# Kernel optimization log

Hardware: AMD Instinct MI355X
Metric: run time of the kernel (lower is better)

Reference implementation:

```python
import jax, jax.numpy as jnp
import numpy as np

N = 50000      # nodes
E = 800000     # edges
H = 64         # num_hidden
NUM_LAYERS = 4 # -> NUM_LAYERS-1 shared-weight processor steps
EPS = 1e-12


def _mlp3(x, w1, b1, w2, b2, w3, b3):
    h = jax.nn.relu(x @ w1 + b1)
    h = jax.nn.relu(h @ w2 + b2)
    return h @ w3 + b3


def setup_inputs() -> dict:
    key = jax.random.key(0)
    ks = jax.random.split(key, 32)

    def gl(k, shape):
        fan_in = shape[0]
        return (jax.random.normal(k, shape, jnp.float32) / np.sqrt(fan_in)).astype(jnp.float32)

    inp = {
        "X_curr": jax.random.normal(ks[0], (N, 6), jnp.float32),
        "y_prev": jax.random.normal(ks[1], (N,), jnp.float32),
        "edge": jax.random.randint(ks[2], (2, E), 0, N, dtype=jnp.int64),
        # edge net: Linear(9,H) ReLU Linear(H,H) ReLU Linear(H,3)
        "ew1": gl(ks[3], (9, H)), "eb1": jnp.zeros((H,), jnp.float32),
        "ew2": gl(ks[4], (H, H)), "eb2": jnp.zeros((H,), jnp.float32),
        "ew3": gl(ks[5], (H, 3)), "eb3": jnp.zeros((3,), jnp.float32),
        # node net: Linear(5,H) ReLU Linear(H,H) ReLU Linear(H,1)
        "nw1": gl(ks[6], (5, H)), "nb1": jnp.zeros((H,), jnp.float32),
        "nw2": gl(ks[7], (H, H)), "nb2": jnp.zeros((H,), jnp.float32),
        "nw3": gl(ks[8], (H, 1)), "nb3": jnp.zeros((1,), jnp.float32),
        # decoder: Linear(5,H) ReLU Linear(H,H) ReLU Linear(H,H) ReLU Linear(H,1)
        "dw1": gl(ks[9], (5, H)),  "db1": jnp.zeros((H,), jnp.float32),
        "dw2": gl(ks[10], (H, H)), "db2": jnp.zeros((H,), jnp.float32),
        "dw3": gl(ks[11], (H, H)), "db3": jnp.zeros((H,), jnp.float32),
        "dw4": gl(ks[12], (H, 1)), "db4": jnp.zeros((1,), jnp.float32),
        "mode": 0,
    }
    return inp


def reference(X_curr, y_prev, edge,
              ew1, eb1, ew2, eb2, ew3, eb3,
              nw1, nb1, nw2, nb2, nw3, nb3,
              dw1, db1, dw2, db2, dw3, db3, dw4, db4,
              mode):
    src, dst = edge[0], edge[1]
    n = X_curr.shape[0]

    # x_in: [N,5] = (pos x,y,z, feature col 4, y_prev)
    x_in = jnp.concatenate([X_curr[:, jnp.array([0, 1, 2, 4])], y_prev[:, None]], axis=-1)

    # initial edge_attr = (f_dest - f_src) * disp  -> [E,3]
    disp0 = x_in[dst, :3] - x_in[src, :3]
    f_r = x_in[dst, 4] - x_in[src, 4]
    edge_attr = f_r[:, None] * disp0

    cnt = jax.ops.segment_sum(jnp.ones((edge.shape[1], 1), x_in.dtype), dst, num_segments=n)
    denom = jnp.maximum(cnt, 1.0)

    for _ in range(NUM_LAYERS - 1):  # shared weights across processors
        xs = x_in[src]
        xd = x_in[dst]
        disp = xd[:, :3] - xs[:, :3]
        norm = jnp.sqrt(jnp.sum(disp * disp, axis=-1, keepdims=True) + EPS)
        net_in = jnp.concatenate([disp, norm, edge_attr, xs[:, 4:5], xd[:, 4:5]], axis=-1)  # [E,9]
        edge_attr = edge_attr + _mlp3(net_in, ew1, eb1, ew2, eb2, ew3, eb3)

        # scatter-mean of edge_attr at destination nodes
        aggr = jax.ops.segment_sum(edge_attr, dst, num_segments=n) / denom  # [N,3]
        node_in = jnp.concatenate([x_in[:, 3:5], aggr], axis=-1)            # [N,5]
        delta = _mlp3(node_in, nw1, nb1, nw2, nb2, nw3, nb3)[:, 0]
        x_in = jnp.concatenate([x_in[:, :4], (x_in[:, 4] + delta)[:, None]], axis=-1)

    # decoder
    h = jax.nn.relu(x_in @ dw1 + db1)
    h = jax.nn.relu(h @ dw2 + db2)
    h = jax.nn.relu(h @ dw3 + db3)
    x_out = h @ dw4 + db4  # [N,1]
    return y_prev + x_out[:, 0]
```

## Files before the change

kernel.cpp:

```cpp
#include <hip/hip_runtime.h>
#include <math.h>

#define N_NODES 50000
#define N_EDGES 800000
#define EPS 1e-12f
#define SCAN_NB 196
#define MAXB 6144

typedef __attribute__((ext_vector_type(8))) short bf16x8;
typedef __attribute__((ext_vector_type(4))) float f32x4;

__device__ inline unsigned pk_bf16(float a, float b) {
    unsigned ua = __float_as_uint(a), ub = __float_as_uint(b);
    ua = (ua + 0x7FFFu + ((ua >> 16) & 1u)) >> 16;
    ub = (ub + 0x7FFFu + ((ub >> 16) & 1u)) >> 16;
    return ua | (ub << 16);
}
__device__ inline unsigned short bf16_1(float a) {
    unsigned ua = __float_as_uint(a);
    return (unsigned short)((ua + 0x7FFFu + ((ua >> 16) & 1u)) >> 16);
}

__global__ void k_node_init(const float* __restrict__ X, const float* __restrict__ yp,
                            float4* __restrict__ px4, float* __restrict__ f) {
    int n = blockIdx.x * blockDim.x + threadIdx.x;
    if (n < N_NODES) {
        px4[n] = make_float4(X[n * 6 + 0], X[n * 6 + 1], X[n * 6 + 2], X[n * 6 + 4]);
        f[n] = yp[n];
    }
}

__global__ __launch_bounds__(256) void k_bucket(const int* __restrict__ edge,
                                                int* __restrict__ btail,
                                                int2* __restrict__ staging) {
    __shared__ int hist[256], loff[256], gbase[256], fill[256];
    __shared__ int2 ebL[2048];
    __shared__ unsigned short bktL[2048];
    const int t = threadIdx.x;
    const int base = blockIdx.x * 2048;
    const int cnt = min(2048, N_EDGES - base);
    hist[t] = 0; fill[t] = 0;
    __syncthreads();

    int2 my[8]; int mb[8];
#pragma unroll
    for (int j = 0; j < 8; j++) {
        int i = base + t + j * 256;
        if (i < N_EDGES) {
            int s = edge[i], d = edge[N_EDGES + i];
            my[j] = make_int2(s, d);
            mb[j] = d >> 8;
            atomicAdd(&hist[mb[j]], 1);
        } else mb[j] = -1;
    }
    __syncthreads();
    int v = hist[t];
    loff[t] = v;
    __syncthreads();
    for (int off = 1; off < 256; off <<= 1) {
        int x = (t >= off) ? loff[t - off] : 0;
        __syncthreads();
        loff[t] += x;
        __syncthreads();
    }
    int ex = loff[t] - v;
    __syncthreads();
    loff[t] = ex;
    if (v > 0) gbase[t] = atomicAdd(&btail[t], v);
    __syncthreads();
#pragma unroll
    for (int j = 0; j < 8; j++) {
        if (mb[j] >= 0) {
            int lp = loff[mb[j]] + atomicAdd(&fill[mb[j]], 1);
            ebL[lp] = my[j];
            bktL[lp] = (unsigned short)mb[j];
        }
    }
    __syncthreads();
    for (int i = t; i < cnt; i += 256) {
        int b = bktL[i];
        int gp = gbase[b] + (i - loff[b]);
        if (gp < MAXB) staging[b * MAXB + gp] = ebL[i];
    }
}

__global__ void k_bscan(const int* __restrict__ btail, int* __restrict__ bbase) {
    __shared__ int s[256];
    int t = threadIdx.x;
    int v = (t < SCAN_NB) ? btail[t] : 0;
    s[t] = v;
    __syncthreads();
    for (int off = 1; off < 256; off <<= 1) {
        int x = (t >= off) ? s[t - off] : 0;
        __syncthreads();
        s[t] += x;
        __syncthreads();
    }
    if (t < SCAN_NB) bbase[t] = s[t] - v;
}

__global__ __launch_bounds__(256) void k_bsort(const int2* __restrict__ staging,
                                               const int* __restrict__ btail,
                                               const int* __restrict__ bbase,
                                               int2* __restrict__ sd,
                                               int* __restrict__ rowptr) {
    __shared__ int hist[256], excl[256], fill[256], sbuf[256];
    __shared__ int2 ebL[MAXB];
    const int b = blockIdx.x, t = threadIdx.x;
    const int size = min(btail[b], MAXB);
    const int gb = bbase[b];
    for (int i = t; i < size; i += 256) ebL[i] = staging[b * MAXB + i];
    hist[t] = 0; fill[t] = 0;
    __syncthreads();
    for (int i = t; i < size; i += 256) atomicAdd(&hist[ebL[i].y & 255], 1);
    __syncthreads();
    int v = hist[t];
    sbuf[t] = v;
    __syncthreads();
    for (int off = 1; off < 256; off <<= 1) {
        int x = (t >= off) ? sbuf[t - off] : 0;
        __syncthreads();
        sbuf[t] += x;
        __syncthreads();
    }
    int ex = sbuf[t] - v;
    excl[t] = ex;
    int n = (b << 8) + t;
    if (n < N_NODES) rowptr[n] = gb + ex;
    if (b == SCAN_NB - 1 && t == 0) rowptr[N_NODES] = N_EDGES;
    __syncthreads();
    for (int i = t; i < size; i += 256) {
        int2 v2 = ebL[i];
        int ld = v2.y & 255;
        int pos = excl[ld] + atomicAdd(&fill[ld], 1);
        sd[gb + pos] = v2;
    }
}

__global__ void k_edge_init(const int2* __restrict__ sd,
                            const float4* __restrict__ px4,
                            const float* __restrict__ yp,
                            float4* __restrict__ dnrm, float4* __restrict__ ea) {
    int e = blockIdx.x * blockDim.x + threadIdx.x;
    if (e < N_EDGES) {
        int2 SD = sd[e];
        float4 ps = px4[SD.x], pd = px4[SD.y];
        float dx = pd.x - ps.x, dy = pd.y - ps.y, dz = pd.z - ps.z;
        float nrm = sqrtf(dx * dx + dy * dy + dz * dz + EPS);
        dnrm[e] = make_float4(dx, dy, dz, nrm);
        float fr = yp[SD.y] - yp[SD.x];
        ea[e] = make_float4(fr * dx, fr * dy, fr * dz, 0.f);
    }
}

#define W1OFF 0
#define W2OFF 4096
#define W3OFF 13312
#define BUFOFF 15616
#define RS 144

__global__ __launch_bounds__(256, 2) void k_edge_mlp(
    const int2* __restrict__ sd, const float4* __restrict__ dnrm,
    float4* __restrict__ ea, const float* __restrict__ f,
    const float* __restrict__ ew1, const float* __restrict__ eb1,
    const float* __restrict__ ew2, const float* __restrict__ eb2,
    const float* __restrict__ ew3, const float* __restrict__ eb3) {
    __shared__ __align__(16) char smem[15616 + 4 * 64 * RS];
    const int t = threadIdx.x;
    const int lane = t & 63, wave = t >> 6;
    const int c = lane & 15, q = lane >> 4;

    {
        int n = t & 63, kg = t >> 6;
        unsigned pk[4];
#pragma unroll
        for (int i = 0; i < 4; i++) {
            int k0 = kg * 8 + i * 2;
            float v0 = (k0 < 9) ? ew1[k0 * 64 + n] : 0.f;
            float v1 = (k0 + 1 < 9) ? ew1[(k0 + 1) * 64 + n] : 0.f;
            pk[i] = pk_bf16(v0, v1);
        }
        *(uint4*)(smem + W1OFF + n * 64 + kg * 16) =
            make_uint4(pk[0], pk[1], pk[2], pk[3]);

        unsigned pk2[8];
#pragma unroll
        for (int i = 0; i < 8; i++) {
            int k0 = kg * 16 + i * 2;
            pk2[i] = pk_bf16(ew2[k0 * 64 + n], ew2[(k0 + 1) * 64 + n]);
        }
        *(uint4*)(smem + W2OFF + n * RS + kg * 32) =
            make_uint4(pk2[0], pk2[1], pk2[2], pk2[3]);
        *(uint4*)(smem + W2OFF + n * RS + kg * 32 + 16) =
            make_uint4(pk2[4], pk2[5], pk2[6], pk2[7]);

        int n3 = t & 15, kg3 = t >> 4;
        unsigned pk3[2];
#pragma unroll
        for (int i = 0; i < 2; i++) {
            int k0 = kg3 * 4 + i * 2;
            float v0 = (n3 < 3) ? ew3[k0 * 3 + n3] : 0.f;
            float v1 = (n3 < 3) ? ew3[(k0 + 1) * 3 + n3] : 0.f;
            pk3[i] = pk_bf16(v0, v1);
        }
        *(uint2*)(smem + W3OFF + n3 * RS + kg3 * 8) = make_uint2(pk3[0], pk3[1]);
    }

    char* mybuf = smem + BUFOFF + wave * (64 * RS);
    const int e = blockIdx.x * 256 + t;
    int2 SD = sd[e];
    float4 DN = dnrm[e];
    float4 EA = ea[e];
    float fs = f[SD.x], fd = f[SD.y];
    {
        char* row = mybuf + lane * RS;
        *(uint4*)(row) = make_uint4(pk_bf16(DN.x, DN.y), pk_bf16(DN.z, DN.w),
                                    pk_bf16(EA.x, EA.y), pk_bf16(EA.z, fs));
        *(uint4*)(row + 16) = make_uint4(pk_bf16(fd, 0.f), 0u, 0u, 0u);
        *(uint4*)(row + 32) = make_uint4(0u, 0u, 0u, 0u);
        *(uint4*)(row + 48) = make_uint4(0u, 0u, 0u, 0u);
    }
    __syncthreads();

    {
        bf16x8 A1[4], B1[4];
#pragma unroll
        for (int mt = 0; mt < 4; mt++)
            A1[mt] = *(bf16x8*)(mybuf + (mt * 16 + c) * RS + q * 16);
#pragma unroll
        for (int nt = 0; nt < 4; nt++)
            B1[nt] = *(bf16x8*)(smem + W1OFF + (nt * 16 + c) * 64 + q * 16);
        f32x4 acc[16];
#pragma unroll
        for (int nt = 0; nt < 4; nt++) {
            float b = eb1[nt * 16 + c];
#pragma unroll
            for (int mt = 0; mt < 4; mt++) acc[mt * 4 + nt] = (f32x4){b, b, b, b};
        }
#pragma unroll
        for (int mt = 0; mt < 4; mt++)
#pragma unroll
            for (int nt = 0; nt < 4; nt++)
                acc[mt * 4 + nt] = __builtin_amdgcn_mfma_f32_16x16x32_bf16(
                    A1[mt], B1[nt], acc[mt * 4 + nt], 0, 0, 0);
#pragma unroll
        for (int mt = 0; mt < 4; mt++)
#pragma unroll
            for (int nt = 0; nt < 4; nt++)
#pragma unroll
                for (int r = 0; r < 4; r++)
                    *(unsigned short*)(mybuf + (mt * 16 + q * 4 + r) * RS +
                                       (nt * 16 + c) * 2) =
                        bf16_1(fmaxf(acc[mt * 4 + nt][r], 0.f));
    }

    bf16x8 B2[8], B3[2];
#pragma unroll
    for (int nt = 0; nt < 4; nt++)
#pragma unroll
        for (int ks = 0; ks < 2; ks++)
            B2[nt * 2 + ks] =
                *(bf16x8*)(smem + W2OFF + (nt * 16 + c) * RS + ks * 64 + q * 16);
#pragma unroll
    for (int ks = 0; ks < 2; ks++)
        B3[ks] = *(bf16x8*)(smem + W3OFF + c * RS + ks * 64 + q * 16);
    float b3i = (c < 3) ? eb3[c] : 0.f;

#pragma unroll
    for (int mt = 0; mt < 4; mt++) {
        bf16x8 A2[2];
#pragma unroll
        for (int ks = 0; ks < 2; ks++)
            A2[ks] = *(bf16x8*)(mybuf + (mt * 16 + c) * RS + ks * 64 + q * 16);
        f32x4 a2[4];
#pragma unroll
        for (int nt = 0; nt < 4; nt++) {
            float b = eb2[nt * 16 + c];
            a2[nt] = (f32x4){b, b, b, b};
            a2[nt] = __builtin_amdgcn_mfma_f32_16x16x32_bf16(A2[0], B2[nt * 2 + 0],
                                                             a2[nt], 0, 0, 0);
            a2[nt] = __builtin_amdgcn_mfma_f32_16x16x32_bf16(A2[1], B2[nt * 2 + 1],
                                                             a2[nt], 0, 0, 0);
        }
#pragma unroll
        for (int nt = 0; nt < 4; nt++)
#pragma unroll
            for (int r = 0; r < 4; r++)
                *(unsigned short*)(mybuf + (mt * 16 + q * 4 + r) * RS +
                                   (nt * 16 + c) * 2) =
                    bf16_1(fmaxf(a2[nt][r], 0.f));
        bf16x8 A3[2];
#pragma unroll
        for (int ks = 0; ks < 2; ks++)
            A3[ks] = *(bf16x8*)(mybuf + (mt * 16 + c) * RS + ks * 64 + q * 16);
        f32x4 a3 = (f32x4){b3i, b3i, b3i, b3i};
        a3 = __builtin_amdgcn_mfma_f32_16x16x32_bf16(A3[0], B3[0], a3, 0, 0, 0);
        a3 = __builtin_amdgcn_mfma_f32_16x16x32_bf16(A3[1], B3[1], a3, 0, 0, 0);
        if (c < 3) {
#pragma unroll
            for (int r = 0; r < 4; r++)
                *(float*)(mybuf + (mt * 16 + q * 4 + r) * RS + 128 + c * 4) = a3[r];
        }
    }

    float4 o = *(float4*)(mybuf + lane * RS + 128);
    ea[e] = make_float4(EA.x + o.x, EA.y + o.y, EA.z + o.z, 0.f);
}

__global__ __launch_bounds__(256, 2) void k_node_mlp(
    const float4* __restrict__ px4, float* __restrict__ f,
    const float4* __restrict__ ea, const int* __restrict__ rowptr,
    const float* __restrict__ nw1, const float* __restrict__ nb1,
    const float* __restrict__ nw2, const float* __restrict__ nb2,
    const float* __restrict__ nw3, const float* __restrict__ nb3) {
    __shared__ __align__(16) char smem[15616 + 4 * 64 * RS];
    const int t = threadIdx.x;
    const int lane = t & 63, wave = t >> 6;
    const int c = lane & 15, q = lane >> 4;

    {
        int n = t & 63, kg = t >> 6;
        unsigned pk[4];
#pragma unroll
        for (int i = 0; i < 4; i++) {
            int k0 = kg * 8 + i * 2;
            float v0 = (k0 < 5) ? nw1[k0 * 64 + n] : 0.f;
            float v1 = (k0 + 1 < 5) ? nw1[(k0 + 1) * 64 + n] : 0.f;
            pk[i] = pk_bf16(v0, v1);
        }
        *(uint4*)(smem + W1OFF + n * 64 + kg * 16) =
            make_uint4(pk[0], pk[1], pk[2], pk[3]);

        unsigned pk2[8];
#pragma unroll
        for (int i = 0; i < 8; i++) {
            int k0 = kg * 16 + i * 2;
            pk2[i] = pk_bf16(nw2[k0 * 64 + n], nw2[(k0 + 1) * 64 + n]);
        }
        *(uint4*)(smem + W2OFF + n * RS + kg * 32) =
            make_uint4(pk2[0], pk2[1], pk2[2], pk2[3]);
        *(uint4*)(smem + W2OFF + n * RS + kg * 32 + 16) =
            make_uint4(pk2[4], pk2[5], pk2[6], pk2[7]);

        int n3 = t & 15, kg3 = t >> 4;
        unsigned pk3[2];
#pragma unroll
        for (int i = 0; i < 2; i++) {
            int k0 = kg3 * 4 + i * 2;
            float v0 = (n3 == 0) ? nw3[k0] : 0.f;
            float v1 = (n3 == 0) ? nw3[k0 + 1] : 0.f;
            pk3[i] = pk_bf16(v0, v1);
        }
        *(uint2*)(smem + W3OFF + n3 * RS + kg3 * 8) = make_uint2(pk3[0], pk3[1]);
    }

    char* mybuf = smem + BUFOFF + wave * (64 * RS);
    const int idx = blockIdx.x * 256 + t;
    const int n = (idx < N_NODES) ? idx : (N_NODES - 1);

    int b0 = rowptr[n], b1 = rowptr[n + 1];
    float a0 = 0.f, a1 = 0.f, a2 = 0.f;
    for (int p = b0; p < b1; p++) {
        float4 v = ea[p];
        a0 += v.x; a1 += v.y; a2 += v.z;
    }
    float inv = 1.0f / fmaxf((float)(b1 - b0), 1.0f);
    float4 P = px4[n];
    float fn = f[n];
    {
        char* row = mybuf + lane * RS;
        *(uint4*)(row) = make_uint4(pk_bf16(P.w, fn), pk_bf16(a0 * inv, a1 * inv),
                                    pk_bf16(a2 * inv, 0.f), 0u);
        *(uint4*)(row + 16) = make_uint4(0u, 0u, 0u, 0u);
        *(uint4*)(row + 32) = make_uint4(0u, 0u, 0u, 0u);
        *(uint4*)(row + 48) = make_uint4(0u, 0u, 0u, 0u);
    }
    __syncthreads();

    {
        bf16x8 A1[4], B1[4];
#pragma unroll
        for (int mt = 0; mt < 4; mt++)
            A1[mt] = *(bf16x8*)(mybuf + (mt * 16 + c) * RS + q * 16);
#pragma unroll
        for (int nt = 0; nt < 4; nt++)
            B1[nt] = *(bf16x8*)(smem + W1OFF + (nt * 16 + c) * 64 + q * 16);
        f32x4 acc[16];
#pragma unroll
        for (int nt = 0; nt < 4; nt++) {
            float b = nb1[nt * 16 + c];
#pragma unroll
            for (int mt = 0; mt < 4; mt++) acc[mt * 4 + nt] = (f32x4){b, b, b, b};
        }
#pragma unroll
        for (int mt = 0; mt < 4; mt++)
#pragma unroll
            for (int nt = 0; nt < 4; nt++)
                acc[mt * 4 + nt] = __builtin_amdgcn_mfma_f32_16x16x32_bf16(
                    A1[mt], B1[nt], acc[mt * 4 + nt], 0, 0, 0);
#pragma unroll
        for (int mt = 0; mt < 4; mt++)
#pragma unroll
            for (int nt = 0; nt < 4; nt++)
#pragma unroll
                for (int r = 0; r < 4; r++)
                    *(unsigned short*)(mybuf + (mt * 16 + q * 4 + r) * RS +
                                       (nt * 16 + c) * 2) =
                        bf16_1(fmaxf(acc[mt * 4 + nt][r], 0.f));
    }

    bf16x8 B2[8], B3[2];
#pragma unroll
    for (int nt = 0; nt < 4; nt++)
#pragma unroll
        for (int ks = 0; ks < 2; ks++)
            B2[nt * 2 + ks] =
                *(bf16x8*)(smem + W2OFF + (nt * 16 + c) * RS + ks * 64 + q * 16);
#pragma unroll
    for (int ks = 0; ks < 2; ks++)
        B3[ks] = *(bf16x8*)(smem + W3OFF + c * RS + ks * 64 + q * 16);
    float b3s = (c == 0) ? nb3[0] : 0.f;

#pragma unroll
    for (int mt = 0; mt < 4; mt++) {
        bf16x8 A2[2];
#pragma unroll
        for (int ks = 0; ks < 2; ks++)
            A2[ks] = *(bf16x8*)(mybuf + (mt * 16 + c) * RS + ks * 64 + q * 16);
        f32x4 a2[4];
#pragma unroll
        for (int nt = 0; nt < 4; nt++) {
            float b = nb2[nt * 16 + c];
            a2[nt] = (f32x4){b, b, b, b};
            a2[nt] = __builtin_amdgcn_mfma_f32_16x16x32_bf16(A2[0], B2[nt * 2 + 0],
                                                             a2[nt], 0, 0, 0);
            a2[nt] = __builtin_amdgcn_mfma_f32_16x16x32_bf16(A2[1], B2[nt * 2 + 1],
                                                             a2[nt], 0, 0, 0);
        }
#pragma unroll
        for (int nt = 0; nt < 4; nt++)
#pragma unroll
            for (int r = 0; r < 4; r++)
                *(unsigned short*)(mybuf + (mt * 16 + q * 4 + r) * RS +
                                   (nt * 16 + c) * 2) =
                    bf16_1(fmaxf(a2[nt][r], 0.f));
        bf16x8 A3[2];
#pragma unroll
        for (int ks = 0; ks < 2; ks++)
            A3[ks] = *(bf16x8*)(mybuf + (mt * 16 + c) * RS + ks * 64 + q * 16);
        f32x4 a3 = (f32x4){b3s, b3s, b3s, b3s};
        a3 = __builtin_amdgcn_mfma_f32_16x16x32_bf16(A3[0], B3[0], a3, 0, 0, 0);
        a3 = __builtin_amdgcn_mfma_f32_16x16x32_bf16(A3[1], B3[1], a3, 0, 0, 0);
        if (c == 0) {
#pragma unroll
            for (int r = 0; r < 4; r++)
                *(float*)(mybuf + (mt * 16 + q * 4 + r) * RS + 128) = a3[r];
        }
    }

    float o = *(float*)(mybuf + lane * RS + 128);
    if (idx < N_NODES) f[n] = fn + o;
}

#define DW1OFF 0
#define DW2OFF 4096
#define DW3OFF 13312
#define DW4OFF 22528
#define DBUFOFF 24832

__global__ __launch_bounds__(256, 2) void k_decoder(
    const float4* __restrict__ px4, const float* __restrict__ f,
    const float* __restrict__ yp,
    const float* __restrict__ dw1, const float* __restrict__ db1,
    const float* __restrict__ dw2, const float* __restrict__ db2,
    const float* __restrict__ dw3, const float* __restrict__ db3,
    const float* __restrict__ dw4, const float* __restrict__ db4,
    float* __restrict__ out) {
    __shared__ __align__(16) char smem[24832 + 4 * 64 * RS];
    const int t = threadIdx.x;
    const int lane = t & 63, wave = t >> 6;
    const int c = lane & 15, q = lane >> 4;

    {
        int n = t & 63, kg = t >> 6;
        unsigned pk[4];
#pragma unroll
        for (int i = 0; i < 4; i++) {
            int k0 = kg * 8 + i * 2;
            float v0 = (k0 < 5) ? dw1[k0 * 64 + n] : 0.f;
            float v1 = (k0 + 1 < 5) ? dw1[(k0 + 1) * 64 + n] : 0.f;
            pk[i] = pk_bf16(v0, v1);
        }
        *(uint4*)(smem + DW1OFF + n * 64 + kg * 16) =
            make_uint4(pk[0], pk[1], pk[2], pk[3]);

        unsigned pk2[8], pk3b[8];
#pragma unroll
        for (int i = 0; i < 8; i++) {
            int k0 = kg * 16 + i * 2;
            pk2[i] = pk_bf16(dw2[k0 * 64 + n], dw2[(k0 + 1) * 64 + n]);
            pk3b[i] = pk_bf16(dw3[k0 * 64 + n], dw3[(k0 + 1) * 64 + n]);
        }
        *(uint4*)(smem + DW2OFF + n * RS + kg * 32) =
            make_uint4(pk2[0], pk2[1], pk2[2], pk2[3]);
        *(uint4*)(smem + DW2OFF + n * RS + kg * 32 + 16) =
            make_uint4(pk2[4], pk2[5], pk2[6], pk2[7]);
        *(uint4*)(smem + DW3OFF + n * RS + kg * 32) =
            make_uint4(pk3b[0], pk3b[1], pk3b[2], pk3b[3]);
        *(uint4*)(smem + DW3OFF + n * RS + kg * 32 + 16) =
            make_uint4(pk3b[4], pk3b[5], pk3b[6], pk3b[7]);

        int n4 = t & 15, kg4 = t >> 4;
        unsigned pk4[2];
#pragma unroll
        for (int i = 0; i < 2; i++) {
            int k0 = kg4 * 4 + i * 2;
            float v0 = (n4 == 0) ? dw4[k0] : 0.f;
            float v1 = (n4 == 0) ? dw4[k0 + 1] : 0.f;
            pk4[i] = pk_bf16(v0, v1);
        }
        *(uint2*)(smem + DW4OFF + n4 * RS + kg4 * 8) = make_uint2(pk4[0], pk4[1]);
    }

    char* mybuf = smem + DBUFOFF + wave * (64 * RS);
    const int idx = blockIdx.x * 256 + t;
    const int n = (idx < N_NODES) ? idx : (N_NODES - 1);
    float4 P = px4[n];
    float fn = f[n];
    {
        char* row = mybuf + lane * RS;
        *(uint4*)(row) = make_uint4(pk_bf16(P.x, P.y), pk_bf16(P.z, P.w),
                                    pk_bf16(fn, 0.f), 0u);
        *(uint4*)(row + 16) = make_uint4(0u, 0u, 0u, 0u);
        *(uint4*)(row + 32) = make_uint4(0u, 0u, 0u, 0u);
        *(uint4*)(row + 48) = make_uint4(0u, 0u, 0u, 0u);
    }
    __syncthreads();

    {
        bf16x8 A1[4], B1[4];
#pragma unroll
        for (int mt = 0; mt < 4; mt++)
            A1[mt] = *(bf16x8*)(mybuf + (mt * 16 + c) * RS + q * 16);
#pragma unroll
        for (int nt = 0; nt < 4; nt++)
            B1[nt] = *(bf16x8*)(smem + DW1OFF + (nt * 16 + c) * 64 + q * 16);
        f32x4 acc[16];
#pragma unroll
        for (int nt = 0; nt < 4; nt++) {
            float b = db1[nt * 16 + c];
#pragma unroll
            for (int mt = 0; mt < 4; mt++) acc[mt * 4 + nt] = (f32x4){b, b, b, b};
        }
#pragma unroll
        for (int mt = 0; mt < 4; mt++)
#pragma unroll
            for (int nt = 0; nt < 4; nt++)
                acc[mt * 4 + nt] = __builtin_amdgcn_mfma_f32_16x16x32_bf16(
                    A1[mt], B1[nt], acc[mt * 4 + nt], 0, 0, 0);
#pragma unroll
        for (int mt = 0; mt < 4; mt++)
#pragma unroll
            for (int nt = 0; nt < 4; nt++)
#pragma unroll
                for (int r = 0; r < 4; r++)
                    *(unsigned short*)(mybuf + (mt * 16 + q * 4 + r) * RS +
                                       (nt * 16 + c) * 2) =
                        bf16_1(fmaxf(acc[mt * 4 + nt][r], 0.f));
    }

    bf16x8 B2[8], B3[8], B4[2];
#pragma unroll
    for (int nt = 0; nt < 4; nt++)
#pragma unroll
        for (int ks = 0; ks < 2; ks++) {
            B2[nt * 2 + ks] =
                *(bf16x8*)(smem + DW2OFF + (nt * 16 + c) * RS + ks * 64 + q * 16);
            B3[nt * 2 + ks] =
                *(bf16x8*)(smem + DW3OFF + (nt * 16 + c) * RS + ks * 64 + q * 16);
        }
#pragma unroll
    for (int ks = 0; ks < 2; ks++)
        B4[ks] = *(bf16x8*)(smem + DW4OFF + c * RS + ks * 64 + q * 16);
    float b4s = (c == 0) ? db4[0] : 0.f;

#pragma unroll
    for (int mt = 0; mt < 4; mt++) {
        bf16x8 A2[2];
#pragma unroll
        for (int ks = 0; ks < 2; ks++)
            A2[ks] = *(bf16x8*)(mybuf + (mt * 16 + c) * RS + ks * 64 + q * 16);
        f32x4 a2[4];
#pragma unroll
        for (int nt = 0; nt < 4; nt++) {
            float b = db2[nt * 16 + c];
            a2[nt] = (f32x4){b, b, b, b};
            a2[nt] = __builtin_amdgcn_mfma_f32_16x16x32_bf16(A2[0], B2[nt * 2 + 0],
                                                             a2[nt], 0, 0, 0);
            a2[nt] = __builtin_amdgcn_mfma_f32_16x16x32_bf16(A2[1], B2[nt * 2 + 1],
                                                             a2[nt], 0, 0, 0);
        }
#pragma unroll
        for (int nt = 0; nt < 4; nt++)
#pragma unroll
            for (int r = 0; r < 4; r++)
                *(unsigned short*)(mybuf + (mt * 16 + q * 4 + r) * RS +
                                   (nt * 16 + c) * 2) =
                    bf16_1(fmaxf(a2[nt][r], 0.f));
        bf16x8 A3[2];
#pragma unroll
        for (int ks = 0; ks < 2; ks++)
            A3[ks] = *(bf16x8*)(mybuf + (mt * 16 + c) * RS + ks * 64 + q * 16);
        f32x4 a3v[4];
#pragma unroll
        for (int nt = 0; nt < 4; nt++) {
            float b = db3[nt * 16 + c];
            a3v[nt] = (f32x4){b, b, b, b};
            a3v[nt] = __builtin_amdgcn_mfma_f32_16x16x32_bf16(A3[0], B3[nt * 2 + 0],
                                                              a3v[nt], 0, 0, 0);
            a3v[nt] = __builtin_amdgcn_mfma_f32_16x16x32_bf16(A3[1], B3[nt * 2 + 1],
                                                              a3v[nt], 0, 0, 0);
        }
#pragma unroll
        for (int nt = 0; nt < 4; nt++)
#pragma unroll
            for (int r = 0; r < 4; r++)
                *(unsigned short*)(mybuf + (mt * 16 + q * 4 + r) * RS +
                                   (nt * 16 + c) * 2) =
                    bf16_1(fmaxf(a3v[nt][r], 0.f));
        bf16x8 A4[2];
#pragma unroll
        for (int ks = 0; ks < 2; ks++)
            A4[ks] = *(bf16x8*)(mybuf + (mt * 16 + c) * RS + ks * 64 + q * 16);
        f32x4 a4 = (f32x4){b4s, b4s, b4s, b4s};
        a4 = __builtin_amdgcn_mfma_f32_16x16x32_bf16(A4[0], B4[0], a4, 0, 0, 0);
        a4 = __builtin_amdgcn_mfma_f32_16x16x32_bf16(A4[1], B4[1], a4, 0, 0, 0);
        if (c == 0) {
#pragma unroll
            for (int r = 0; r < 4; r++)
                *(float*)(mybuf + (mt * 16 + q * 4 + r) * RS + 128) = a4[r];
        }
    }

    float o = *(float*)(mybuf + lane * RS + 128);
    if (idx < N_NODES) out[n] = yp[n] + o;
}

extern "C" void kernel_launch(void* const* d_in, const int* in_sizes, int n_in,
                              void* d_out, int out_size, void* d_ws, size_t ws_size,
                              hipStream_t stream) {
    const float* X    = (const float*)d_in[0];
    const float* yp   = (const float*)d_in[1];
    const int*   edge = (const int*)d_in[2];
    const float *ew1 = (const float*)d_in[3],  *eb1 = (const float*)d_in[4];
    const float *ew2 = (const float*)d_in[5],  *eb2 = (const float*)d_in[6];
    const float *ew3 = (const float*)d_in[7],  *eb3 = (const float*)d_in[8];
    const float *nw1 = (const float*)d_in[9],  *nb1 = (const float*)d_in[10];
    const float *nw2 = (const float*)d_in[11], *nb2 = (const float*)d_in[12];
    const float *nw3 = (const float*)d_in[13], *nb3 = (const float*)d_in[14];
    const float *dw1 = (const float*)d_in[15], *db1 = (const float*)d_in[16];
    const float *dw2 = (const float*)d_in[17], *db2 = (const float*)d_in[18];
    const float *dw3 = (const float*)d_in[19], *db3 = (const float*)d_in[20];
    const float *dw4 = (const float*)d_in[21], *db4 = (const float*)d_in[22];
    float* out = (float*)d_out;

    char* p = (char*)d_ws;
    auto carve = [&](size_t bytes) {
        char* r = p;
        p += (bytes + 255) & ~(size_t)255;
        return r;
    };
    int2*   sd     = (int2*)  carve(sizeof(int2)   * N_EDGES);
    float4* dnrm   = (float4*)carve(sizeof(float4) * N_EDGES);
    float4* ea     = (float4*)carve(sizeof(float4) * N_EDGES);
    float4* px4    = (float4*)carve(sizeof(float4) * N_NODES);
    float*  f      = (float*) carve(sizeof(float)  * N_NODES);
    int*    rowptr = (int*)   carve(sizeof(int)    * (N_NODES + 1));
    int*    btail  = (int*)   carve(sizeof(int)    * 256);
    int*    bbase  = (int*)   carve(sizeof(int)    * 256);
    int2*   staging = (int2*)dnrm;

    const int nb_n = SCAN_NB;
    const int nb_e = (N_EDGES + 255) / 256;
    const int nb_b = (N_EDGES + 2047) / 2048;

    hipMemsetAsync(btail, 0, sizeof(int) * 256, stream);
    k_node_init<<<nb_n, 256, 0, stream>>>(X, yp, px4, f);
    k_bucket<<<nb_b, 256, 0, stream>>>(edge, btail, staging);
    k_bscan<<<1, 256, 0, stream>>>(btail, bbase);
    k_bsort<<<SCAN_NB, 256, 0, stream>>>(staging, btail, bbase, sd, rowptr);
    k_edge_init<<<nb_e, 256, 0, stream>>>(sd, px4, yp, dnrm, ea);

    for (int it = 0; it < 3; ++it) {
        k_edge_mlp<<<nb_e, 256, 0, stream>>>(sd, dnrm, ea, f,
                                             ew1, eb1, ew2, eb2, ew3, eb3);
        k_node_mlp<<<nb_n, 256, 0, stream>>>(px4, f, ea, rowptr,
                                             nw1, nb1, nw2, nb2, nw3, nb3);
    }
    k_decoder<<<nb_n, 256, 0, stream>>>(px4, f, yp,
                                        dw1, db1, dw2, db2, dw3, db3, dw4, db4, out);
}
```

Before: 295.5 us.

## Fuse scatter-mean aggregation into edge MLP via block segmented reduce and atomics

The edge MLP kernel now reduces its updated edge attributes per destination node inside each block, which works because edges are sorted by destination. A leader thread per run of equal destinations issues atomic adds into a new per-node aggregate buffer. The node MLP then reads the three sums directly instead of looping over each node's CSR edge range. This removes the per-node serial gather over edge attributes, at the cost of a memset per iteration, extra block-wide syncs, shared-memory reuse and float atomics with nondeterministic summation order.

```diff
diff --git a/kernel.cpp b/kernel.cpp
--- a/kernel.cpp
+++ b/kernel.cpp
@@ -164,7 +164,8 @@
     float4* __restrict__ ea, const float* __restrict__ f,
     const float* __restrict__ ew1, const float* __restrict__ eb1,
     const float* __restrict__ ew2, const float* __restrict__ eb2,
-    const float* __restrict__ ew3, const float* __restrict__ eb3) {
+    const float* __restrict__ ew3, const float* __restrict__ eb3,
+    float* __restrict__ aggr) {
     __shared__ __align__(16) char smem[15616 + 4 * 64 * RS];
     const int t = threadIdx.x;
     const int lane = t & 63, wave = t >> 6;
@@ -302,14 +303,35 @@
                 *(float*)(mybuf + (mt * 16 + q * 4 + r) * RS + 128 + c * 4) = a3[r];
         }
     }
+    __syncthreads();
 
     float4 o = *(float4*)(mybuf + lane * RS + 128);
-    ea[e] = make_float4(EA.x + o.x, EA.y + o.y, EA.z + o.z, 0.f);
+    float r0 = EA.x + o.x, r1 = EA.y + o.y, r2 = EA.z + o.z;
+    ea[e] = make_float4(r0, r1, r2, 0.f);
+
+    int* dstL = (int*)(smem + W1OFF);
+    float4* resL = (float4*)(smem + W1OFF + 1024);
+    dstL[t] = SD.y;
+    resL[t] = make_float4(r0, r1, r2, 0.f);
+    __syncthreads();
+    bool leader = (t == 0) || (dstL[t - 1] != SD.y);
+    if (leader) {
+        float s0 = 0.f, s1 = 0.f, s2 = 0.f;
+        int j = t;
+        while (j < 256 && dstL[j] == SD.y) {
+            float4 v = resL[j];
+            s0 += v.x; s1 += v.y; s2 += v.z;
+            j++;
+        }
+        atomicAdd(&aggr[SD.y * 3 + 0], s0);
+        atomicAdd(&aggr[SD.y * 3 + 1], s1);
+        atomicAdd(&aggr[SD.y * 3 + 2], s2);
+    }
 }
 
 __global__ __launch_bounds__(256, 2) void k_node_mlp(
     const float4* __restrict__ px4, float* __restrict__ f,
-    const float4* __restrict__ ea, const int* __restrict__ rowptr,
+    const float* __restrict__ aggr, const int* __restrict__ rowptr,
     const float* __restrict__ nw1, const float* __restrict__ nb1,
     const float* __restrict__ nw2, const float* __restrict__ nb2,
     const float* __restrict__ nw3, const float* __restrict__ nb3) {
@@ -358,19 +380,16 @@
     const int idx = blockIdx.x * 256 + t;
     const int n = (idx < N_NODES) ? idx : (N_NODES - 1);
 
-    int b0 = rowptr[n], b1 = rowptr[n + 1];
-    float a0 = 0.f, a1 = 0.f, a2 = 0.f;
-    for (int p = b0; p < b1; p++) {
-        float4 v = ea[p];
-        a0 += v.x; a1 += v.y; a2 += v.z;
-    }
-    float inv = 1.0f / fmaxf((float)(b1 - b0), 1.0f);
+    int deg = rowptr[n + 1] - rowptr[n];
+    float inv = 1.0f / fmaxf((float)deg, 1.0f);
+    float a0 = aggr[n * 3 + 0] * inv, a1 = aggr[n * 3 + 1] * inv,
+          a2 = aggr[n * 3 + 2] * inv;
     float4 P = px4[n];
     float fn = f[n];
     {
         char* row = mybuf + lane * RS;
-        *(uint4*)(row) = make_uint4(pk_bf16(P.w, fn), pk_bf16(a0 * inv, a1 * inv),
-                                    pk_bf16(a2 * inv, 0.f), 0u);
+        *(uint4*)(row) = make_uint4(pk_bf16(P.w, fn), pk_bf16(a0, a1),
+                                    pk_bf16(a2, 0.f), 0u);
         *(uint4*)(row + 16) = make_uint4(0u, 0u, 0u, 0u);
         *(uint4*)(row + 32) = make_uint4(0u, 0u, 0u, 0u);
         *(uint4*)(row + 48) = make_uint4(0u, 0u, 0u, 0u);
@@ -675,6 +694,7 @@
     float4* ea     = (float4*)carve(sizeof(float4) * N_EDGES);
     float4* px4    = (float4*)carve(sizeof(float4) * N_NODES);
     float*  f      = (float*) carve(sizeof(float)  * N_NODES);
+    float*  aggr   = (float*) carve(sizeof(float)  * 3 * N_NODES);
     int*    rowptr = (int*)   carve(sizeof(int)    * (N_NODES + 1));
     int*    btail  = (int*)   carve(sizeof(int)    * 256);
     int*    bbase  = (int*)   carve(sizeof(int)    * 256);
@@ -692,9 +712,10 @@
     k_edge_init<<<nb_e, 256, 0, stream>>>(sd, px4, yp, dnrm, ea);
 
     for (int it = 0; it < 3; ++it) {
+        hipMemsetAsync(aggr, 0, sizeof(float) * 3 * N_NODES, stream);
         k_edge_mlp<<<nb_e, 256, 0, stream>>>(sd, dnrm, ea, f,
-                                             ew1, eb1, ew2, eb2, ew3, eb3);
-        k_node_mlp<<<nb_n, 256, 0, stream>>>(px4, f, ea, rowptr,
+                                             ew1, eb1, ew2, eb2, ew3, eb3, aggr);
+        k_node_mlp<<<nb_n, 256, 0, stream>>>(px4, f, aggr, rowptr,
                                              nw1, nb1, nw2, nb2, nw3, nb3);
     }
     k_decoder<<<nb_n, 256, 0, stream>>>(px4, f, yp,
```

Result: slower. 317.0 us (+7.3%).
